# Kernel optimization log

Measured on AMD Instinct MI355X. Metric: run time of the kernel, lower is better.

The kernel has to match this reference:

```python
import jax, jax.numpy as jnp
import numpy as np

EPS = 1e-08


def setup_inputs() -> dict:
    key = jax.random.key(0)
    k1, k2 = jax.random.split(key)
    query_features = jax.random.normal(k1, (64, 1024, 32, 32), dtype=jnp.float32)
    support_features = jax.random.normal(k2, (25, 1024, 32, 32), dtype=jnp.float32)
    return {"query_features": query_features, "support_features": support_features}


def reference(query_features, support_features):
    B, C, h, w = support_features.shape
    NQ = query_features.shape[0]
    # Covariance over channels: flatten support to (C, B*h*w), center, GEMM.
    support = jnp.transpose(support_features, (1, 0, 2, 3)).reshape(C, -1)
    centered = support - jnp.mean(support, axis=1, keepdims=True)
    N = B * h * w
    cov = (centered @ centered.T) / (N - 1 + EPS)  # (C, C)
    # Queries: (NQ, C, d), L2-normalize each channel row over spatial dim.
    q = query_features.reshape(NQ, C, -1)
    q = q / (jnp.linalg.norm(q, axis=2, keepdims=True) + EPS)
    # diag(q^T cov q) without materializing (d, d): cov@q then elementwise reduce over C.
    cq = jnp.einsum('cD,nDd->ncd', cov, q)  # (NQ, C, d)
    scores = jnp.mean(jnp.sum(q * cq, axis=1), axis=1)  # (NQ,)
    return scores
```

## Files before the change

### kernel.cpp

```cpp
#include <hip/hip_runtime.h>

#define NQ   64
#define CCH  1024
#define DSP  1024
#define NSUP 25600
#define KSLICES 8
#define NK_COV 50

typedef __attribute__((ext_vector_type(4))) float f32x4;
typedef __attribute__((ext_vector_type(8))) __bf16 bf16x8;

#define WAITVM(N) asm volatile("s_waitcnt vmcnt(" #N ")" ::: "memory")
#define WAITLGKM0() asm volatile("s_waitcnt lgkmcnt(0)" ::: "memory")
#define BAR() __builtin_amdgcn_s_barrier()
#define SCHED0() __builtin_amdgcn_sched_barrier(0)

__device__ inline unsigned short f2bf(float x) {
  unsigned u = __builtin_bit_cast(unsigned, x);
  u += 0x7fffu + ((u >> 16) & 1u);
  return (unsigned short)(u >> 16);
}

__global__ __launch_bounds__(256) void zero_kernel(float4* __restrict__ cov4,
                                                   float4* __restrict__ out4) {
  const int i = blockIdx.x * 256 + threadIdx.x;
  cov4[i] = make_float4(0.f, 0.f, 0.f, 0.f);
  if (i < 16) out4[i] = make_float4(0.f, 0.f, 0.f, 0.f);
}


__global__ __launch_bounds__(512) void mean_center_kernel(
    const float* __restrict__ sup, float* __restrict__ mean,
    unsigned short* __restrict__ Sb, int write_sb) {
  __shared__ float4 row[6400];
  __shared__ float red[512];
  const int c = blockIdx.x;
  const int tid = threadIdx.x;
  float s = 0.f;
  for (int qd = tid; qd < 6400; qd += 512) {
    const int b = qd >> 8, s4 = (qd & 255) << 2;
    const float4 v = *(const float4*)(sup + ((size_t)b * CCH + c) * DSP + s4);
    row[qd] = v;
    s += v.x + v.y + v.z + v.w;
  }
  red[tid] = s;
  __syncthreads();
  for (int st = 256; st > 0; st >>= 1) {
    if (tid < st) red[tid] += red[tid + st];
    __syncthreads();
  }
  const float m = red[0] * (1.0f / 25600.0f);
  if (tid == 0) mean[c] = m;
  if (write_sb) {
    for (int qd = tid; qd < 6400; qd += 512) {
      const float4 v = row[qd];
      const int b = qd >> 8, s4 = (qd & 255) << 2;
      ushort4 o;
      o.x = f2bf(v.x - m); o.y = f2bf(v.y - m);
      o.z = f2bf(v.z - m); o.w = f2bf(v.w - m);
      *(ushort4*)(Sb + (size_t)c * NSUP + b * DSP + s4) = o;
    }
  }
}

__global__ __launch_bounds__(256) void qnorm_kernel(
    const float* __restrict__ q, float* __restrict__ qfac,
    unsigned short* __restrict__ Qb, int write_qb) {
  const int row = blockIdx.x * 4 + (threadIdx.x >> 6);
  const int l = threadIdx.x & 63;
  const float4* src = (const float4*)(q + (size_t)row * DSP);
  float4 v[4];
  float ss = 0.f;
#pragma unroll
  for (int i = 0; i < 4; ++i) {
    v[i] = src[l + 64 * i];
    ss += v[i].x * v[i].x + v[i].y * v[i].y + v[i].z * v[i].z + v[i].w * v[i].w;
  }
#pragma unroll
  for (int off = 32; off > 0; off >>= 1) ss += __shfl_xor(ss, off);
  const float f = 1.0f / (sqrtf(ss) + 1e-8f);
  if (l == 0) qfac[row] = f;
  if (write_qb) {
#pragma unroll
    for (int i = 0; i < 4; ++i) {
      ushort4 o;
      o.x = f2bf(v[i].x * f); o.y = f2bf(v[i].y * f);
      o.z = f2bf(v[i].z * f); o.w = f2bf(v[i].w * f);
      *(ushort4*)(Qb + (size_t)row * DSP + (size_t)(l + 64 * i) * 4) = o;
    }
  }
}


__device__ inline void stage_glds(const unsigned short* __restrict__ src, int ld,
                                  int row0, int k0, unsigned short* lds) {
  const int tid = threadIdx.x;
  const int w = tid >> 6;
#pragma unroll
  for (int it = 0; it < 4; ++it) {
    const int ci = it * 256 + tid;
    const int r = ci >> 3;
    const int kc = ((ci & 7) ^ (r & 7)) << 3;
    const unsigned short* g = src + (size_t)(row0 + r) * ld + k0 + kc;
    unsigned short* lb = lds + ((it * 256 + w * 64) << 3);
    __builtin_amdgcn_global_load_lds((const __attribute__((address_space(1))) void*)g,
                                     (__attribute__((address_space(3))) void*)lb,
                                     16, 0, 0);
  }
}

__device__ inline void stage256(const unsigned short* __restrict__ src,
                                int row0, int k0, unsigned short* lds_base) {
  const int tid = threadIdx.x;
  const int wid = tid >> 6;
#pragma unroll
  for (int it = 0; it < 4; ++it) {
    const int ci = it * 512 + tid;
    const int r = ci >> 3;
    const int kc = ((ci & 7) ^ (r & 7)) << 3;
    const unsigned short* g = src + (size_t)(row0 + r) * DSP + k0 + kc;
    unsigned short* lb = lds_base + ((it * 512 + (wid << 6)) << 3);
    __builtin_amdgcn_global_load_lds((const __attribute__((address_space(1))) void*)g,
                                     (__attribute__((address_space(3))) void*)lb,
                                     16, 0, 0);
  }
}

__device__ inline void rd4(const unsigned short* base, int r0, int col, int lr, bf16x8 f[4]) {
#pragma unroll
  for (int i = 0; i < 4; ++i)
    f[i] = *(const bf16x8*)(const void*)(base + (r0 + i * 16 + lr) * 64 + col);
}
__device__ inline void mfma16(const bf16x8 a[4], const bf16x8 b[4], f32x4 (*acc)[4]) {
  __builtin_amdgcn_s_setprio(1);
#pragma unroll
  for (int i = 0; i < 4; ++i)
#pragma unroll
    for (int j = 0; j < 4; ++j)
      acc[i][j] = __builtin_amdgcn_mfma_f32_16x16x32_bf16(a[i], b[j], acc[i][j], 0, 0, 0);
  __builtin_amdgcn_s_setprio(0);
}

__device__ inline void stage_sup_f32(const float* __restrict__ sup,
                                     const float* __restrict__ mean,
                                     int row0, int k0, unsigned short* lds) {
  const int tid = threadIdx.x;
#pragma unroll
  for (int it = 0; it < 4; ++it) {
    const int ci = it * 256 + tid;
    const int r = ci >> 3, kc = (ci & 7) << 3;
    const int c = row0 + r;
    const int k = k0 + kc;
    const int b = k >> 10, sp = k & 1023;
    const float4* g = (const float4*)(sup + ((size_t)b * CCH + c) * DSP + sp);
    const float4 v0 = g[0], v1 = g[1];
    const float m = mean[c];
    union { unsigned short h[8]; int4 q; } pk;
    pk.h[0] = f2bf(v0.x - m); pk.h[1] = f2bf(v0.y - m);
    pk.h[2] = f2bf(v0.z - m); pk.h[3] = f2bf(v0.w - m);
    pk.h[4] = f2bf(v1.x - m); pk.h[5] = f2bf(v1.y - m);
    pk.h[6] = f2bf(v1.z - m); pk.h[7] = f2bf(v1.w - m);
    *(int4*)(lds + (size_t)(r * 8 + ((ci & 7) ^ (r & 7))) * 8) = pk.q;
  }
}
__device__ inline void stage_q_f32(const float* __restrict__ qn,
                                   const float* __restrict__ qfacn,
                                   int row0, int k0, unsigned short* lds) {
  const int tid = threadIdx.x;
#pragma unroll
  for (int it = 0; it < 4; ++it) {
    const int ci = it * 256 + tid;
    const int r = ci >> 3, kc = (ci & 7) << 3;
    const int c = row0 + r;
    const float4* g = (const float4*)(qn + (size_t)c * DSP + k0 + kc);
    const float4 v0 = g[0], v1 = g[1];
    const float f = qfacn[c];
    union { unsigned short h[8]; int4 q; } pk;
    pk.h[0] = f2bf(v0.x * f); pk.h[1] = f2bf(v0.y * f);
    pk.h[2] = f2bf(v0.z * f); pk.h[3] = f2bf(v0.w * f);
    pk.h[4] = f2bf(v1.x * f); pk.h[5] = f2bf(v1.y * f);
    pk.h[6] = f2bf(v1.z * f); pk.h[7] = f2bf(v1.w * f);
    *(int4*)(lds + (size_t)(r * 8 + ((ci & 7) ^ (r & 7))) * 8) = pk.q;
  }
}
__device__ inline void compute_step(const unsigned short* lA, const unsigned short* lB,
                                    int wr, int wc, int lr, int kg, f32x4 acc[4][4]) {
  const int sc = (lr & 7) << 3;
#pragma unroll
  for (int kk = 0; kk < 64; kk += 32) {
    const int col = (kk + kg) ^ sc;
    bf16x8 a[4], b[4];
    rd4(lA, wr, col, lr, a);
    rd4(lB, wc, col, lr, b);
    mfma16(a, b, (f32x4(*)[4])acc);
#pragma unroll
    for (int i = 0; i < 4; ++i)
#pragma unroll
      for (int j = 0; j < 4; ++j) (void)0;
  }
}

__device__ inline void decode_tile(int t, int& ti, int& tj) {
  int rem = t; ti = 0;
  while (rem >= 8 - ti) { rem -= 8 - ti; ++ti; }
  tj = ti + rem;
}

template <bool F32>
__global__ __launch_bounds__(256) void cov_kernel(
    const unsigned short* __restrict__ Sb, const float* __restrict__ sup,
    const float* __restrict__ mean, float* __restrict__ cov) {
  __shared__ unsigned short clds[32768];
  const int wg = blockIdx.x;
  const int ks = wg & 7;
  int ti, tj; decode_tile(wg >> 3, ti, tj);
  const bool diag = (ti == tj);
  const int tid = threadIdx.x, l = tid & 63, w = tid >> 6;
  const int wr = (w >> 1) * 64, wc = (w & 1) * 64, lr = l & 15, kg = (l >> 4) * 8;
  const int sw = (lr & 7) << 3;
  f32x4 acc[4][4];
#pragma unroll
  for (int i = 0; i < 4; ++i)
#pragma unroll
    for (int j = 0; j < 4; ++j) acc[i][j] = 0.f;

  const int kbase = ks * (NSUP / KSLICES);

  if (F32) {
    unsigned short* lA0 = clds;
    stage_sup_f32(sup, mean, ti * 128, kbase, lA0);
    if (!diag) stage_sup_f32(sup, mean, tj * 128, kbase, lA0 + 8192);
    __syncthreads();
    for (int kt = 0; kt < NK_COV; ++kt) {
      const int cb = (kt & 1) * 16384;
      const int nb = cb ^ 16384;
      if (kt + 1 < NK_COV) {
        const int k1 = kbase + (kt + 1) * 64;
        stage_sup_f32(sup, mean, ti * 128, k1, clds + nb);
        if (!diag) stage_sup_f32(sup, mean, tj * 128, k1, clds + nb + 8192);
      }
      compute_step(clds + cb, diag ? clds + cb : clds + cb + 8192, wr, wc, lr, kg, acc);
      __syncthreads();
    }
  } else {
    stage_glds(Sb, NSUP, ti * 128, kbase, clds);
    if (!diag) stage_glds(Sb, NSUP, tj * 128, kbase, clds + 8192);
    stage_glds(Sb, NSUP, ti * 128, kbase + 64, clds + 16384);
    if (!diag) stage_glds(Sb, NSUP, tj * 128, kbase + 64, clds + 16384 + 8192);
    for (int t = 0; t < NK_COV; ++t) {
      const int cb = (t & 1) * 16384;
      if (t < NK_COV - 1) { if (diag) { WAITVM(4); } else { WAITVM(8); } }
      else { WAITVM(0); }
      BAR(); SCHED0();
      const unsigned short* A = clds + cb;
      const unsigned short* B = diag ? A : A + 8192;
      bf16x8 a[4], b[4];
      {
        const int col = kg ^ sw;
        rd4(A, wr, col, lr, a);
        rd4(B, wc, col, lr, b);
        mfma16(a, b, (f32x4(*)[4])acc);
      }
      {
        const int col = (32 + kg) ^ sw;
        rd4(A, wr, col, lr, a);
        rd4(B, wc, col, lr, b);
        WAITLGKM0();
        BAR(); SCHED0();
        if (t + 2 < NK_COV) {
          const int k2 = kbase + (t + 2) * 64;
          stage_glds(Sb, NSUP, ti * 128, k2, clds + cb);
          if (!diag) stage_glds(Sb, NSUP, tj * 128, k2, clds + cb + 8192);
        }
        mfma16(a, b, (f32x4(*)[4])acc);
      }
    }
  }

  const float scale = 1.0f / (25599.0f + 1e-8f);
  const int rbase = ti * 128 + wr + (l >> 4) * 4;
  const int cbase = tj * 128 + wc + (l & 15);
#pragma unroll
  for (int i = 0; i < 4; ++i)
#pragma unroll
    for (int j = 0; j < 4; ++j)
#pragma unroll
      for (int r = 0; r < 4; ++r)
        atomicAdd(&cov[(size_t)(rbase + i * 16 + r) * CCH + cbase + j * 16],
                  acc[i][j][r] * scale);
}

__global__ __launch_bounds__(256) void gram_kernel_f32(
    const float* __restrict__ q, const float* __restrict__ qfac,
    const float* __restrict__ cov, float* __restrict__ out) {
  __shared__ unsigned short lA[2][128 * 64];
  __shared__ unsigned short lB[2][128 * 64];
  const int wg = blockIdx.x;
  const int xcd = wg & 7, slot = wg >> 3;
  const int n = xcd * 8 + slot / 36;
  int ti, tj; decode_tile(slot % 36, ti, tj);
  const bool diag = (ti == tj);
  const int tid = threadIdx.x, l = tid & 63, w = tid >> 6;
  const int wr = (w >> 1) * 64, wc = (w & 1) * 64, lr = l & 15, kg = (l >> 4) * 8;
  f32x4 acc[4][4];
#pragma unroll
  for (int i = 0; i < 4; ++i)
#pragma unroll
    for (int j = 0; j < 4; ++j) acc[i][j] = 0.f;

  const float* qn = q + (size_t)n * CCH * DSP;
  const float* qfacn = qfac + (size_t)n * CCH;

  stage_q_f32(qn, qfacn, ti * 128, 0, lA[0]);
  if (!diag) stage_q_f32(qn, qfacn, tj * 128, 0, lB[0]);
  __syncthreads();
  int cur = 0;
  for (int kt = 0; kt < 16; ++kt) {
    if (kt + 1 < 16) {
      const int k1 = (kt + 1) * 64;
      stage_q_f32(qn, qfacn, ti * 128, k1, lA[cur ^ 1]);
      if (!diag) stage_q_f32(qn, qfacn, tj * 128, k1, lB[cur ^ 1]);
    }
    compute_step(lA[cur], diag ? lA[cur] : lB[cur], wr, wc, lr, kg, acc);
    __syncthreads();
    cur ^= 1;
  }

  float s = 0.f;
  const int rbase = ti * 128 + wr + (l >> 4) * 4;
  const int cbase = tj * 128 + wc + (l & 15);
#pragma unroll
  for (int i = 0; i < 4; ++i)
#pragma unroll
    for (int j = 0; j < 4; ++j)
#pragma unroll
      for (int r = 0; r < 4; ++r)
        s += acc[i][j][r] * cov[(size_t)(rbase + i * 16 + r) * CCH + cbase + j * 16];
  if (!diag) s *= 2.0f;
  s *= (1.0f / 1024.0f);
#pragma unroll
  for (int off = 32; off > 0; off >>= 1) s += __shfl_xor(s, off);
  if (l == 0) atomicAdd(&out[n], s);
}

__global__ __launch_bounds__(512, 2) void gram256_kernel(
    const unsigned short* __restrict__ Qb, const float* __restrict__ cov,
    float* __restrict__ out) {
  __shared__ unsigned short lds[65536];
  const int wg = blockIdx.x;
  const int xcd = wg & 7, slot = wg >> 3;
  const int n = xcd * 8 + slot / 10;
  int rem = slot % 10, ti = 0;
  while (rem >= 4 - ti) { rem -= 4 - ti; ++ti; }
  const int tj = ti + rem;
  const bool diag = (ti == tj);
  const int tid = threadIdx.x, l = tid & 63, wid = tid >> 6;
  const int wm = wid >> 2, wn = wid & 3;
  const int lr = l & 15, kg = (l >> 4) * 8;
  const int sw = (lr & 7) << 3;
  const unsigned short* Qn = Qb + (size_t)n * CCH * DSP;

  f32x4 acc[8][4];
#pragma unroll
  for (int i = 0; i < 8; ++i)
#pragma unroll
    for (int j = 0; j < 4; ++j) acc[i][j] = 0.f;

  stage256(Qn, ti * 256, 0, lds);
  if (!diag) stage256(Qn, tj * 256, 0, lds + 16384);
  stage256(Qn, ti * 256, 64, lds + 32768);
  if (!diag) stage256(Qn, tj * 256, 64, lds + 32768 + 16384);

  for (int t = 0; t < 16; ++t) {
    const int cb = (t & 1) << 15;
    if (t < 15) { if (diag) { WAITVM(4); } else { WAITVM(8); } }
    else { WAITVM(0); }
    BAR(); SCHED0();
    const unsigned short* A = lds + cb + wm * 8192;
    const unsigned short* B = lds + cb + (diag ? 0 : 16384) + (wn >> 1) * 8192;
    const int brow = (wn & 1) * 64;
    bf16x8 a[4], b[4];
    {
      const int col = kg ^ sw;
      rd4(B, brow, col, lr, b);
      rd4(A, 0, col, lr, a);
      mfma16(a, b, &acc[0]);
      rd4(A, 64, col, lr, a);
      mfma16(a, b, &acc[4]);
    }
    {
      const int col = (32 + kg) ^ sw;
      rd4(B, brow, col, lr, b);
      rd4(A, 0, col, lr, a);
      mfma16(a, b, &acc[0]);
      rd4(A, 64, col, lr, a);
      WAITLGKM0();
      BAR(); SCHED0();
      if (t + 2 < 16) {
        stage256(Qn, ti * 256, (t + 2) * 64, lds + cb);
        if (!diag) stage256(Qn, tj * 256, (t + 2) * 64, lds + cb + 16384);
      }
      mfma16(a, b, &acc[4]);
    }
  }

  float s = 0.f;
  const int rbase = ti * 256 + wm * 128 + (l >> 4) * 4;
  const int cbase = tj * 256 + wn * 64 + (l & 15);
#pragma unroll
  for (int i = 0; i < 8; ++i)
#pragma unroll
    for (int j = 0; j < 4; ++j)
#pragma unroll
      for (int r = 0; r < 4; ++r)
        s += acc[i][j][r] * cov[(size_t)(rbase + i * 16 + r) * CCH + cbase + j * 16];
  if (!diag) s *= 2.0f;
  s *= (1.0f / 1024.0f);
#pragma unroll
  for (int off = 32; off > 0; off >>= 1) s += __shfl_xor(s, off);
  if (l == 0) atomicAdd(&out[n], s);
}

extern "C" void kernel_launch(void* const* d_in, const int* in_sizes, int n_in,
                              void* d_out, int out_size, void* d_ws, size_t ws_size,
                              hipStream_t stream) {
  const float* q = (const float*)d_in[0];
  const float* sup = (const float*)d_in[1];
  float* out = (float*)d_out;

  char* ws = (char*)d_ws;
  float* mean = (float*)ws;
  float* qfac = (float*)(ws + (4 << 10));
  float* cov  = (float*)(ws + (4 << 10) + (256 << 10));
  unsigned short* Sb = (unsigned short*)(ws + (4 << 10) + (256 << 10) + (4 << 20));
  unsigned short* Qb = Sb + (size_t)CCH * NSUP;
  const size_t need_fat = (size_t)(4 << 10) + (256 << 10) + (4 << 20) +
                          (size_t)CCH * NSUP * 2 + (size_t)NQ * CCH * DSP * 2;
  const bool fat = ws_size >= need_fat;

  zero_kernel<<<1024, 256, 0, stream>>>((float4*)cov, (float4*)out);

  mean_center_kernel<<<CCH, 512, 0, stream>>>(sup, mean, Sb, fat ? 1 : 0);
  qnorm_kernel<<<NQ * CCH / 4, 256, 0, stream>>>(q, qfac, Qb, fat ? 1 : 0);

  if (fat) {
    cov_kernel<false><<<dim3(288), 256, 0, stream>>>(Sb, sup, mean, cov);
    gram256_kernel<<<dim3(640), 512, 0, stream>>>(Qb, cov, out);
  } else {
    cov_kernel<true><<<dim3(288), 256, 0, stream>>>(Sb, sup, mean, cov);
    gram_kernel_f32<<<dim3(8 * 8 * 36), 256, 0, stream>>>(q, qfac, cov, out);
  }
}
```

Baseline: 270.4 us.

## Use 256x256 tiles for covariance GEMM and split-K the Gram kernel

The covariance GEMM moves from a 128x128-tile, 8-way split-K kernel to the 512-thread 256x256-tile pipelined loop already used by the Gram kernel, with 25 K-slices of 1024 over 10 upper-triangular tile pairs. The Gram kernel is split into two K-halves, doubling its grid to 1280 workgroups so more CUs stay busy. The shared loop is factored into a templated helper. In exchange there are more atomics into cov and out, and the covariance grid launches a few idle workgroups.

```diff
diff --git a/kernel.cpp b/kernel.cpp
--- a/kernel.cpp
+++ b/kernel.cpp
@@ -4,8 +4,6 @@
 #define CCH  1024
 #define DSP  1024
 #define NSUP 25600
-#define KSLICES 8
-#define NK_COV 50
 
 typedef __attribute__((ext_vector_type(4))) float f32x4;
 typedef __attribute__((ext_vector_type(8))) __bf16 bf16x8;
@@ -92,25 +90,24 @@
 }
 
 
-__device__ inline void stage_glds(const unsigned short* __restrict__ src, int ld,
-                                  int row0, int k0, unsigned short* lds) {
-  const int tid = threadIdx.x;
-  const int w = tid >> 6;
-#pragma unroll
-  for (int it = 0; it < 4; ++it) {
-    const int ci = it * 256 + tid;
-    const int r = ci >> 3;
-    const int kc = ((ci & 7) ^ (r & 7)) << 3;
-    const unsigned short* g = src + (size_t)(row0 + r) * ld + k0 + kc;
-    unsigned short* lb = lds + ((it * 256 + w * 64) << 3);
-    __builtin_amdgcn_global_load_lds((const __attribute__((address_space(1))) void*)g,
-                                     (__attribute__((address_space(3))) void*)lb,
-                                     16, 0, 0);
-  }
-}
-
-__device__ inline void stage256(const unsigned short* __restrict__ src,
-                                int row0, int k0, unsigned short* lds_base) {
+__device__ inline void rd4(const unsigned short* base, int r0, int col, int lr, bf16x8 f[4]) {
+#pragma unroll
+  for (int i = 0; i < 4; ++i)
+    f[i] = *(const bf16x8*)(const void*)(base + (r0 + i * 16 + lr) * 64 + col);
+}
+__device__ inline void mfma16(const bf16x8 a[4], const bf16x8 b[4], f32x4 (*acc)[4]) {
+  __builtin_amdgcn_s_setprio(1);
+#pragma unroll
+  for (int i = 0; i < 4; ++i)
+#pragma unroll
+    for (int j = 0; j < 4; ++j)
+      acc[i][j] = __builtin_amdgcn_mfma_f32_16x16x32_bf16(a[i], b[j], acc[i][j], 0, 0, 0);
+  __builtin_amdgcn_s_setprio(0);
+}
+
+
+__device__ inline void stage256g(const unsigned short* __restrict__ src, int ld,
+                                 int row0, int k0, unsigned short* lds_base) {
   const int tid = threadIdx.x;
   const int wid = tid >> 6;
 #pragma unroll
@@ -118,7 +115,7 @@
     const int ci = it * 512 + tid;
     const int r = ci >> 3;
     const int kc = ((ci & 7) ^ (r & 7)) << 3;
-    const unsigned short* g = src + (size_t)(row0 + r) * DSP + k0 + kc;
+    const unsigned short* g = src + (size_t)(row0 + r) * ld + k0 + kc;
     unsigned short* lb = lds_base + ((it * 512 + (wid << 6)) << 3);
     __builtin_amdgcn_global_load_lds((const __attribute__((address_space(1))) void*)g,
                                      (__attribute__((address_space(3))) void*)lb,
@@ -126,254 +123,20 @@
   }
 }
 
-__device__ inline void rd4(const unsigned short* base, int r0, int col, int lr, bf16x8 f[4]) {
-#pragma unroll
-  for (int i = 0; i < 4; ++i)
-    f[i] = *(const bf16x8*)(const void*)(base + (r0 + i * 16 + lr) * 64 + col);
-}
-__device__ inline void mfma16(const bf16x8 a[4], const bf16x8 b[4], f32x4 (*acc)[4]) {
-  __builtin_amdgcn_s_setprio(1);
-#pragma unroll
-  for (int i = 0; i < 4; ++i)
-#pragma unroll
-    for (int j = 0; j < 4; ++j)
-      acc[i][j] = __builtin_amdgcn_mfma_f32_16x16x32_bf16(a[i], b[j], acc[i][j], 0, 0, 0);
-  __builtin_amdgcn_s_setprio(0);
-}
-
-__device__ inline void stage_sup_f32(const float* __restrict__ sup,
-                                     const float* __restrict__ mean,
-                                     int row0, int k0, unsigned short* lds) {
-  const int tid = threadIdx.x;
-#pragma unroll
-  for (int it = 0; it < 4; ++it) {
-    const int ci = it * 256 + tid;
-    const int r = ci >> 3, kc = (ci & 7) << 3;
-    const int c = row0 + r;
-    const int k = k0 + kc;
-    const int b = k >> 10, sp = k & 1023;
-    const float4* g = (const float4*)(sup + ((size_t)b * CCH + c) * DSP + sp);
-    const float4 v0 = g[0], v1 = g[1];
-    const float m = mean[c];
-    union { unsigned short h[8]; int4 q; } pk;
-    pk.h[0] = f2bf(v0.x - m); pk.h[1] = f2bf(v0.y - m);
-    pk.h[2] = f2bf(v0.z - m); pk.h[3] = f2bf(v0.w - m);
-    pk.h[4] = f2bf(v1.x - m); pk.h[5] = f2bf(v1.y - m);
-    pk.h[6] = f2bf(v1.z - m); pk.h[7] = f2bf(v1.w - m);
-    *(int4*)(lds + (size_t)(r * 8 + ((ci & 7) ^ (r & 7))) * 8) = pk.q;
-  }
-}
-__device__ inline void stage_q_f32(const float* __restrict__ qn,
-                                   const float* __restrict__ qfacn,
-                                   int row0, int k0, unsigned short* lds) {
-  const int tid = threadIdx.x;
-#pragma unroll
-  for (int it = 0; it < 4; ++it) {
-    const int ci = it * 256 + tid;
-    const int r = ci >> 3, kc = (ci & 7) << 3;
-    const int c = row0 + r;
-    const float4* g = (const float4*)(qn + (size_t)c * DSP + k0 + kc);
-    const float4 v0 = g[0], v1 = g[1];
-    const float f = qfacn[c];
-    union { unsigned short h[8]; int4 q; } pk;
-    pk.h[0] = f2bf(v0.x * f); pk.h[1] = f2bf(v0.y * f);
-    pk.h[2] = f2bf(v0.z * f); pk.h[3] = f2bf(v0.w * f);
-    pk.h[4] = f2bf(v1.x * f); pk.h[5] = f2bf(v1.y * f);
-    pk.h[6] = f2bf(v1.z * f); pk.h[7] = f2bf(v1.w * f);
-    *(int4*)(lds + (size_t)(r * 8 + ((ci & 7) ^ (r & 7))) * 8) = pk.q;
-  }
-}
-__device__ inline void compute_step(const unsigned short* lA, const unsigned short* lB,
-                                    int wr, int wc, int lr, int kg, f32x4 acc[4][4]) {
-  const int sc = (lr & 7) << 3;
-#pragma unroll
-  for (int kk = 0; kk < 64; kk += 32) {
-    const int col = (kk + kg) ^ sc;
-    bf16x8 a[4], b[4];
-    rd4(lA, wr, col, lr, a);
-    rd4(lB, wc, col, lr, b);
-    mfma16(a, b, (f32x4(*)[4])acc);
-#pragma unroll
-    for (int i = 0; i < 4; ++i)
-#pragma unroll
-      for (int j = 0; j < 4; ++j) (void)0;
-  }
-}
-
-__device__ inline void decode_tile(int t, int& ti, int& tj) {
-  int rem = t; ti = 0;
-  while (rem >= 8 - ti) { rem -= 8 - ti; ++ti; }
-  tj = ti + rem;
-}
-
-template <bool F32>
-__global__ __launch_bounds__(256) void cov_kernel(
-    const unsigned short* __restrict__ Sb, const float* __restrict__ sup,
-    const float* __restrict__ mean, float* __restrict__ cov) {
-  __shared__ unsigned short clds[32768];
-  const int wg = blockIdx.x;
-  const int ks = wg & 7;
-  int ti, tj; decode_tile(wg >> 3, ti, tj);
-  const bool diag = (ti == tj);
-  const int tid = threadIdx.x, l = tid & 63, w = tid >> 6;
-  const int wr = (w >> 1) * 64, wc = (w & 1) * 64, lr = l & 15, kg = (l >> 4) * 8;
-  const int sw = (lr & 7) << 3;
-  f32x4 acc[4][4];
-#pragma unroll
-  for (int i = 0; i < 4; ++i)
-#pragma unroll
-    for (int j = 0; j < 4; ++j) acc[i][j] = 0.f;
-
-  const int kbase = ks * (NSUP / KSLICES);
-
-  if (F32) {
-    unsigned short* lA0 = clds;
-    stage_sup_f32(sup, mean, ti * 128, kbase, lA0);
-    if (!diag) stage_sup_f32(sup, mean, tj * 128, kbase, lA0 + 8192);
-    __syncthreads();
-    for (int kt = 0; kt < NK_COV; ++kt) {
-      const int cb = (kt & 1) * 16384;
-      const int nb = cb ^ 16384;
-      if (kt + 1 < NK_COV) {
-        const int k1 = kbase + (kt + 1) * 64;
-        stage_sup_f32(sup, mean, ti * 128, k1, clds + nb);
-        if (!diag) stage_sup_f32(sup, mean, tj * 128, k1, clds + nb + 8192);
-      }
-      compute_step(clds + cb, diag ? clds + cb : clds + cb + 8192, wr, wc, lr, kg, acc);
-      __syncthreads();
-    }
-  } else {
-    stage_glds(Sb, NSUP, ti * 128, kbase, clds);
-    if (!diag) stage_glds(Sb, NSUP, tj * 128, kbase, clds + 8192);
-    stage_glds(Sb, NSUP, ti * 128, kbase + 64, clds + 16384);
-    if (!diag) stage_glds(Sb, NSUP, tj * 128, kbase + 64, clds + 16384 + 8192);
-    for (int t = 0; t < NK_COV; ++t) {
-      const int cb = (t & 1) * 16384;
-      if (t < NK_COV - 1) { if (diag) { WAITVM(4); } else { WAITVM(8); } }
-      else { WAITVM(0); }
-      BAR(); SCHED0();
-      const unsigned short* A = clds + cb;
-      const unsigned short* B = diag ? A : A + 8192;
-      bf16x8 a[4], b[4];
-      {
-        const int col = kg ^ sw;
-        rd4(A, wr, col, lr, a);
-        rd4(B, wc, col, lr, b);
-        mfma16(a, b, (f32x4(*)[4])acc);
-      }
-      {
-        const int col = (32 + kg) ^ sw;
-        rd4(A, wr, col, lr, a);
-        rd4(B, wc, col, lr, b);
-        WAITLGKM0();
-        BAR(); SCHED0();
-        if (t + 2 < NK_COV) {
-          const int k2 = kbase + (t + 2) * 64;
-          stage_glds(Sb, NSUP, ti * 128, k2, clds + cb);
-          if (!diag) stage_glds(Sb, NSUP, tj * 128, k2, clds + cb + 8192);
-        }
-        mfma16(a, b, (f32x4(*)[4])acc);
-      }
-    }
-  }
-
-  const float scale = 1.0f / (25599.0f + 1e-8f);
-  const int rbase = ti * 128 + wr + (l >> 4) * 4;
-  const int cbase = tj * 128 + wc + (l & 15);
-#pragma unroll
-  for (int i = 0; i < 4; ++i)
-#pragma unroll
-    for (int j = 0; j < 4; ++j)
-#pragma unroll
-      for (int r = 0; r < 4; ++r)
-        atomicAdd(&cov[(size_t)(rbase + i * 16 + r) * CCH + cbase + j * 16],
-                  acc[i][j][r] * scale);
-}
-
-__global__ __launch_bounds__(256) void gram_kernel_f32(
-    const float* __restrict__ q, const float* __restrict__ qfac,
-    const float* __restrict__ cov, float* __restrict__ out) {
-  __shared__ unsigned short lA[2][128 * 64];
-  __shared__ unsigned short lB[2][128 * 64];
-  const int wg = blockIdx.x;
-  const int xcd = wg & 7, slot = wg >> 3;
-  const int n = xcd * 8 + slot / 36;
-  int ti, tj; decode_tile(slot % 36, ti, tj);
-  const bool diag = (ti == tj);
-  const int tid = threadIdx.x, l = tid & 63, w = tid >> 6;
-  const int wr = (w >> 1) * 64, wc = (w & 1) * 64, lr = l & 15, kg = (l >> 4) * 8;
-  f32x4 acc[4][4];
-#pragma unroll
-  for (int i = 0; i < 4; ++i)
-#pragma unroll
-    for (int j = 0; j < 4; ++j) acc[i][j] = 0.f;
-
-  const float* qn = q + (size_t)n * CCH * DSP;
-  const float* qfacn = qfac + (size_t)n * CCH;
-
-  stage_q_f32(qn, qfacn, ti * 128, 0, lA[0]);
-  if (!diag) stage_q_f32(qn, qfacn, tj * 128, 0, lB[0]);
-  __syncthreads();
-  int cur = 0;
-  for (int kt = 0; kt < 16; ++kt) {
-    if (kt + 1 < 16) {
-      const int k1 = (kt + 1) * 64;
-      stage_q_f32(qn, qfacn, ti * 128, k1, lA[cur ^ 1]);
-      if (!diag) stage_q_f32(qn, qfacn, tj * 128, k1, lB[cur ^ 1]);
-    }
-    compute_step(lA[cur], diag ? lA[cur] : lB[cur], wr, wc, lr, kg, acc);
-    __syncthreads();
-    cur ^= 1;
-  }
-
-  float s = 0.f;
-  const int rbase = ti * 128 + wr + (l >> 4) * 4;
-  const int cbase = tj * 128 + wc + (l & 15);
-#pragma unroll
-  for (int i = 0; i < 4; ++i)
-#pragma unroll
-    for (int j = 0; j < 4; ++j)
-#pragma unroll
-      for (int r = 0; r < 4; ++r)
-        s += acc[i][j][r] * cov[(size_t)(rbase + i * 16 + r) * CCH + cbase + j * 16];
-  if (!diag) s *= 2.0f;
-  s *= (1.0f / 1024.0f);
-#pragma unroll
-  for (int off = 32; off > 0; off >>= 1) s += __shfl_xor(s, off);
-  if (l == 0) atomicAdd(&out[n], s);
-}
-
-__global__ __launch_bounds__(512, 2) void gram256_kernel(
-    const unsigned short* __restrict__ Qb, const float* __restrict__ cov,
-    float* __restrict__ out) {
-  __shared__ unsigned short lds[65536];
-  const int wg = blockIdx.x;
-  const int xcd = wg & 7, slot = wg >> 3;
-  const int n = xcd * 8 + slot / 10;
-  int rem = slot % 10, ti = 0;
-  while (rem >= 4 - ti) { rem -= 4 - ti; ++ti; }
-  const int tj = ti + rem;
-  const bool diag = (ti == tj);
-  const int tid = threadIdx.x, l = tid & 63, wid = tid >> 6;
-  const int wm = wid >> 2, wn = wid & 3;
-  const int lr = l & 15, kg = (l >> 4) * 8;
-  const int sw = (lr & 7) << 3;
-  const unsigned short* Qn = Qb + (size_t)n * CCH * DSP;
-
-  f32x4 acc[8][4];
-#pragma unroll
-  for (int i = 0; i < 8; ++i)
-#pragma unroll
-    for (int j = 0; j < 4; ++j) acc[i][j] = 0.f;
-
-  stage256(Qn, ti * 256, 0, lds);
-  if (!diag) stage256(Qn, tj * 256, 0, lds + 16384);
-  stage256(Qn, ti * 256, 64, lds + 32768);
-  if (!diag) stage256(Qn, tj * 256, 64, lds + 32768 + 16384);
-
-  for (int t = 0; t < 16; ++t) {
+template <int NT>
+__device__ inline void loop256(const unsigned short* __restrict__ src, int ld,
+                               int rowA, int rowB, int k0, bool diag,
+                               unsigned short* lds,
+                               int wm, int wn, int lr, int kg, int sw,
+                               f32x4 (*acc)[4]) {
+  stage256g(src, ld, rowA, k0, lds);
+  if (!diag) stage256g(src, ld, rowB, k0, lds + 16384);
+  stage256g(src, ld, rowA, k0 + 64, lds + 32768);
+  if (!diag) stage256g(src, ld, rowB, k0 + 64, lds + 32768 + 16384);
+
+  for (int t = 0; t < NT; ++t) {
     const int cb = (t & 1) << 15;
-    if (t < 15) { if (diag) { WAITVM(4); } else { WAITVM(8); } }
+    if (t < NT - 1) { if (diag) { WAITVM(4); } else { WAITVM(8); } }
     else { WAITVM(0); }
     BAR(); SCHED0();
     const unsigned short* A = lds + cb + wm * 8192;
@@ -396,19 +159,253 @@
       rd4(A, 64, col, lr, a);
       WAITLGKM0();
       BAR(); SCHED0();
-      if (t + 2 < 16) {
-        stage256(Qn, ti * 256, (t + 2) * 64, lds + cb);
-        if (!diag) stage256(Qn, tj * 256, (t + 2) * 64, lds + cb + 16384);
+      if (t + 2 < NT) {
+        stage256g(src, ld, rowA, k0 + (t + 2) * 64, lds + cb);
+        if (!diag) stage256g(src, ld, rowB, k0 + (t + 2) * 64, lds + cb + 16384);
       }
       mfma16(a, b, &acc[4]);
     }
   }
+}
+
+__device__ inline void decode_pair4(int p, int& ti, int& tj) {
+  int rem = p; ti = 0;
+  while (rem >= 4 - ti) { rem -= 4 - ti; ++ti; }
+  tj = ti + rem;
+}
+
+__global__ __launch_bounds__(512, 2) void cov256_kernel(
+    const unsigned short* __restrict__ Sb, float* __restrict__ cov) {
+  __shared__ unsigned short lds[65536];
+  const int wg = blockIdx.x;
+  const int g = (wg & 7) * 32 + (wg >> 3);
+  if (g >= 250) return;
+  const int ks = g / 10;
+  int ti, tj; decode_pair4(g % 10, ti, tj);
+  const bool diag = (ti == tj);
+  const int tid = threadIdx.x, l = tid & 63, wid = tid >> 6;
+  const int wm = wid >> 2, wn = wid & 3;
+  const int lr = l & 15, kg = (l >> 4) * 8;
+  const int sw = (lr & 7) << 3;
+
+  f32x4 acc[8][4];
+#pragma unroll
+  for (int i = 0; i < 8; ++i)
+#pragma unroll
+    for (int j = 0; j < 4; ++j) acc[i][j] = 0.f;
+
+  loop256<16>(Sb, NSUP, ti * 256, tj * 256, ks * 1024, diag, lds,
+              wm, wn, lr, kg, sw, acc);
+
+  const float scale = 1.0f / (25599.0f + 1e-8f);
+  const int rbase = ti * 256 + wm * 128 + (l >> 4) * 4;
+  const int cbase = tj * 256 + wn * 64 + (l & 15);
+#pragma unroll
+  for (int i = 0; i < 8; ++i)
+#pragma unroll
+    for (int j = 0; j < 4; ++j)
+#pragma unroll
+      for (int r = 0; r < 4; ++r)
+        atomicAdd(&cov[(size_t)(rbase + i * 16 + r) * CCH + cbase + j * 16],
+                  acc[i][j][r] * scale);
+}
+
+__global__ __launch_bounds__(512, 2) void gram256_kernel(
+    const unsigned short* __restrict__ Qb, const float* __restrict__ cov,
+    float* __restrict__ out) {
+  __shared__ unsigned short lds[65536];
+  const int wg = blockIdx.x;
+  const int xcd = wg & 7, slot = wg >> 3;
+  const int n = xcd * 8 + slot / 20;
+  const int sub = slot % 20;
+  const int kh = sub & 1;
+  int ti, tj; decode_pair4(sub >> 1, ti, tj);
+  const bool diag = (ti == tj);
+  const int tid = threadIdx.x, l = tid & 63, wid = tid >> 6;
+  const int wm = wid >> 2, wn = wid & 3;
+  const int lr = l & 15, kg = (l >> 4) * 8;
+  const int sw = (lr & 7) << 3;
+  const unsigned short* Qn = Qb + (size_t)n * CCH * DSP;
+
+  f32x4 acc[8][4];
+#pragma unroll
+  for (int i = 0; i < 8; ++i)
+#pragma unroll
+    for (int j = 0; j < 4; ++j) acc[i][j] = 0.f;
+
+  loop256<8>(Qn, DSP, ti * 256, tj * 256, kh * 512, diag, lds,
+             wm, wn, lr, kg, sw, acc);
 
   float s = 0.f;
   const int rbase = ti * 256 + wm * 128 + (l >> 4) * 4;
   const int cbase = tj * 256 + wn * 64 + (l & 15);
 #pragma unroll
   for (int i = 0; i < 8; ++i)
+#pragma unroll
+    for (int j = 0; j < 4; ++j)
+#pragma unroll
+      for (int r = 0; r < 4; ++r)
+        s += acc[i][j][r] * cov[(size_t)(rbase + i * 16 + r) * CCH + cbase + j * 16];
+  if (!diag) s *= 2.0f;
+  s *= (1.0f / 1024.0f);
+#pragma unroll
+  for (int off = 32; off > 0; off >>= 1) s += __shfl_xor(s, off);
+  if (l == 0) atomicAdd(&out[n], s);
+}
+
+__device__ inline void mfma16s(const bf16x8 a[4], const bf16x8 b[4], f32x4 acc[4][4]) {
+#pragma unroll
+  for (int i = 0; i < 4; ++i)
+#pragma unroll
+    for (int j = 0; j < 4; ++j)
+      acc[i][j] = __builtin_amdgcn_mfma_f32_16x16x32_bf16(a[i], b[j], acc[i][j], 0, 0, 0);
+}
+
+__device__ inline void stage_sup_f32(const float* __restrict__ sup,
+                                     const float* __restrict__ mean,
+                                     int row0, int k0, unsigned short* lds) {
+  const int tid = threadIdx.x;
+#pragma unroll
+  for (int it = 0; it < 4; ++it) {
+    const int ci = it * 256 + tid;
+    const int r = ci >> 3, kc = (ci & 7) << 3;
+    const int c = row0 + r;
+    const int k = k0 + kc;
+    const int b = k >> 10, sp = k & 1023;
+    const float4* gp = (const float4*)(sup + ((size_t)b * CCH + c) * DSP + sp);
+    const float4 v0 = gp[0], v1 = gp[1];
+    const float m = mean[c];
+    union { unsigned short h[8]; int4 q; } pk;
+    pk.h[0] = f2bf(v0.x - m); pk.h[1] = f2bf(v0.y - m);
+    pk.h[2] = f2bf(v0.z - m); pk.h[3] = f2bf(v0.w - m);
+    pk.h[4] = f2bf(v1.x - m); pk.h[5] = f2bf(v1.y - m);
+    pk.h[6] = f2bf(v1.z - m); pk.h[7] = f2bf(v1.w - m);
+    *(int4*)(lds + (size_t)(r * 8 + ((ci & 7) ^ (r & 7))) * 8) = pk.q;
+  }
+}
+__device__ inline void stage_q_f32(const float* __restrict__ qn,
+                                   const float* __restrict__ qfacn,
+                                   int row0, int k0, unsigned short* lds) {
+  const int tid = threadIdx.x;
+#pragma unroll
+  for (int it = 0; it < 4; ++it) {
+    const int ci = it * 256 + tid;
+    const int r = ci >> 3, kc = (ci & 7) << 3;
+    const int c = row0 + r;
+    const float4* gp = (const float4*)(qn + (size_t)c * DSP + k0 + kc);
+    const float4 v0 = gp[0], v1 = gp[1];
+    const float f = qfacn[c];
+    union { unsigned short h[8]; int4 q; } pk;
+    pk.h[0] = f2bf(v0.x * f); pk.h[1] = f2bf(v0.y * f);
+    pk.h[2] = f2bf(v0.z * f); pk.h[3] = f2bf(v0.w * f);
+    pk.h[4] = f2bf(v1.x * f); pk.h[5] = f2bf(v1.y * f);
+    pk.h[6] = f2bf(v1.z * f); pk.h[7] = f2bf(v1.w * f);
+    *(int4*)(lds + (size_t)(r * 8 + ((ci & 7) ^ (r & 7))) * 8) = pk.q;
+  }
+}
+__device__ inline void compute_step(const unsigned short* lA, const unsigned short* lB,
+                                    int wr, int wc, int lr, int kg, f32x4 acc[4][4]) {
+  const int sc = (lr & 7) << 3;
+#pragma unroll
+  for (int kk = 0; kk < 64; kk += 32) {
+    const int col = (kk + kg) ^ sc;
+    bf16x8 a[4], b[4];
+    rd4(lA, wr, col, lr, a);
+    rd4(lB, wc, col, lr, b);
+    mfma16s(a, b, acc);
+  }
+}
+__device__ inline void decode_tile8(int t, int& ti, int& tj) {
+  int rem = t; ti = 0;
+  while (rem >= 8 - ti) { rem -= 8 - ti; ++ti; }
+  tj = ti + rem;
+}
+
+__global__ __launch_bounds__(256) void cov_kernel_f32(
+    const float* __restrict__ sup, const float* __restrict__ mean,
+    float* __restrict__ cov) {
+  __shared__ unsigned short clds[32768];
+  const int wg = blockIdx.x;
+  const int ks = wg & 7;
+  int ti, tj; decode_tile8(wg >> 3, ti, tj);
+  const bool diag = (ti == tj);
+  const int tid = threadIdx.x, l = tid & 63, w = tid >> 6;
+  const int wr = (w >> 1) * 64, wc = (w & 1) * 64, lr = l & 15, kg = (l >> 4) * 8;
+  f32x4 acc[4][4];
+#pragma unroll
+  for (int i = 0; i < 4; ++i)
+#pragma unroll
+    for (int j = 0; j < 4; ++j) acc[i][j] = 0.f;
+
+  const int kbase = ks * (NSUP / 8);
+  stage_sup_f32(sup, mean, ti * 128, kbase, clds);
+  if (!diag) stage_sup_f32(sup, mean, tj * 128, kbase, clds + 8192);
+  __syncthreads();
+  for (int kt = 0; kt < 50; ++kt) {
+    const int cb = (kt & 1) * 16384;
+    const int nb = cb ^ 16384;
+    if (kt + 1 < 50) {
+      const int k1 = kbase + (kt + 1) * 64;
+      stage_sup_f32(sup, mean, ti * 128, k1, clds + nb);
+      if (!diag) stage_sup_f32(sup, mean, tj * 128, k1, clds + nb + 8192);
+    }
+    compute_step(clds + cb, diag ? clds + cb : clds + cb + 8192, wr, wc, lr, kg, acc);
+    __syncthreads();
+  }
+  const float scale = 1.0f / (25599.0f + 1e-8f);
+  const int rbase = ti * 128 + wr + (l >> 4) * 4;
+  const int cbase = tj * 128 + wc + (l & 15);
+#pragma unroll
+  for (int i = 0; i < 4; ++i)
+#pragma unroll
+    for (int j = 0; j < 4; ++j)
+#pragma unroll
+      for (int r = 0; r < 4; ++r)
+        atomicAdd(&cov[(size_t)(rbase + i * 16 + r) * CCH + cbase + j * 16],
+                  acc[i][j][r] * scale);
+}
+
+__global__ __launch_bounds__(256) void gram_kernel_f32(
+    const float* __restrict__ q, const float* __restrict__ qfac,
+    const float* __restrict__ cov, float* __restrict__ out) {
+  __shared__ unsigned short lA[2][128 * 64];
+  __shared__ unsigned short lB[2][128 * 64];
+  const int wg = blockIdx.x;
+  const int xcd = wg & 7, slot = wg >> 3;
+  const int n = xcd * 8 + slot / 36;
+  int ti, tj; decode_tile8(slot % 36, ti, tj);
+  const bool diag = (ti == tj);
+  const int tid = threadIdx.x, l = tid & 63, w = tid >> 6;
+  const int wr = (w >> 1) * 64, wc = (w & 1) * 64, lr = l & 15, kg = (l >> 4) * 8;
+  f32x4 acc[4][4];
+#pragma unroll
+  for (int i = 0; i < 4; ++i)
+#pragma unroll
+    for (int j = 0; j < 4; ++j) acc[i][j] = 0.f;
+
+  const float* qn = q + (size_t)n * CCH * DSP;
+  const float* qfacn = qfac + (size_t)n * CCH;
+
+  stage_q_f32(qn, qfacn, ti * 128, 0, lA[0]);
+  if (!diag) stage_q_f32(qn, qfacn, tj * 128, 0, lB[0]);
+  __syncthreads();
+  int cur = 0;
+  for (int kt = 0; kt < 16; ++kt) {
+    if (kt + 1 < 16) {
+      const int k1 = (kt + 1) * 64;
+      stage_q_f32(qn, qfacn, ti * 128, k1, lA[cur ^ 1]);
+      if (!diag) stage_q_f32(qn, qfacn, tj * 128, k1, lB[cur ^ 1]);
+    }
+    compute_step(lA[cur], diag ? lA[cur] : lB[cur], wr, wc, lr, kg, acc);
+    __syncthreads();
+    cur ^= 1;
+  }
+
+  float s = 0.f;
+  const int rbase = ti * 128 + wr + (l >> 4) * 4;
+  const int cbase = tj * 128 + wc + (l & 15);
+#pragma unroll
+  for (int i = 0; i < 4; ++i)
 #pragma unroll
     for (int j = 0; j < 4; ++j)
 #pragma unroll
@@ -444,10 +441,10 @@
   qnorm_kernel<<<NQ * CCH / 4, 256, 0, stream>>>(q, qfac, Qb, fat ? 1 : 0);
 
   if (fat) {
-    cov_kernel<false><<<dim3(288), 256, 0, stream>>>(Sb, sup, mean, cov);
-    gram256_kernel<<<dim3(640), 512, 0, stream>>>(Qb, cov, out);
+    cov256_kernel<<<dim3(256), 512, 0, stream>>>(Sb, cov);
+    gram256_kernel<<<dim3(1280), 512, 0, stream>>>(Qb, cov, out);
   } else {
-    cov_kernel<true><<<dim3(288), 256, 0, stream>>>(Sb, sup, mean, cov);
+    cov_kernel_f32<<<dim3(288), 256, 0, stream>>>(sup, mean, cov);
     gram_kernel_f32<<<dim3(8 * 8 * 36), 256, 0, stream>>>(q, qfac, cov, out);
   }
 }
```

New measurement: 301.6 us. 11.5% more time.
